# Kernel tuning notes

Measured on AMD Instinct MI355X. Metric: run time of the kernel, lower is better.

Reference implementation:

```python
import jax, jax.numpy as jnp
import numpy as np

BETA = 0.1
CODEBOOK_SIZE = 32768
EMBED_DIM = 4


def setup_inputs() -> dict:
    key = jax.random.key(0)
    kx, ke = jax.random.split(key)
    x = jax.random.normal(kx, (1, 2, EMBED_DIM, 64, 64), dtype=jnp.float32)
    # codebook init mirrors uniform(-1/K, 1/K) but scale doesn't affect correctness;
    # use normal scaled small to keep distances well-conditioned
    E = jax.random.uniform(ke, (CODEBOOK_SIZE, EMBED_DIM), dtype=jnp.float32,
                           minval=-1.0 / CODEBOOK_SIZE, maxval=1.0 / CODEBOOK_SIZE)
    return {"x": x, "E": E}


def reference(x, E):
    b, t, c, h, w = x.shape
    # (B,T,C,H,W) -> (N, C) with N = B*T*H*W
    x_flat = jnp.transpose(x, (0, 1, 3, 4, 2)).reshape(-1, c)
    d = (jnp.sum(x_flat * x_flat, axis=1, keepdims=True)
         + jnp.sum(E * E, axis=1)
         - 2.0 * jnp.einsum('nc,kc->nk', x_flat, E))
    codes = jnp.argmin(d, axis=1)                      # (N,)
    z_q = E[codes].reshape(b, t, h, w, c)              # gather
    z_q = jnp.transpose(z_q, (0, 1, 4, 2, 3))          # (B,T,C,H,W)
    # commitment + codebook loss
    qloss = (jnp.mean((jax.lax.stop_gradient(z_q) - x) ** 2)
             + BETA * jnp.mean((z_q - jax.lax.stop_gradient(x)) ** 2))
    # straight-through estimator
    z_q_st = x + jax.lax.stop_gradient(z_q - x)
    codes = codes.reshape(b, t, h, w)
    return z_q_st, qloss, codes
```

## Files before the change

kernel.cpp:

```cpp
#include <hip/hip_runtime.h>
#include <cfloat>

#define KC    32768
#define NPTS  8192
#define TPB   256
#define PPT   8
#define PTS_PER_BLK (TPB * PPT)
#define NPB   (NPTS / PTS_PER_BLK)
#define NC    256
#define CHUNK (KC / NC)

typedef float v2f __attribute__((ext_vector_type(2)));

template<int H> __device__ __forceinline__ v2f pk_mul_sg(double a, v2f b) {
    v2f d;
    if constexpr (H == 0)
        asm("v_pk_mul_f32 %0, %1, %2 op_sel:[0,0] op_sel_hi:[0,1]" : "=v"(d) : "s"(a), "v"(b));
    else
        asm("v_pk_mul_f32 %0, %1, %2 op_sel:[1,0] op_sel_hi:[1,1]" : "=v"(d) : "s"(a), "v"(b));
    return d;
}
template<int H> __device__ __forceinline__ v2f pk_fma_sg(double a, v2f b, v2f c) {
    v2f d;
    if constexpr (H == 0)
        asm("v_pk_fma_f32 %0, %1, %2, %3 op_sel:[0,0,0] op_sel_hi:[0,1,1]" : "=v"(d) : "s"(a), "v"(b), "v"(c));
    else
        asm("v_pk_fma_f32 %0, %1, %2, %3 op_sel:[1,0,0] op_sel_hi:[1,1,1]" : "=v"(d) : "s"(a), "v"(b), "v"(c));
    return d;
}
template<int H> __device__ __forceinline__ v2f pk_add_sg(double a, v2f b) {
    v2f d;
    if constexpr (H == 0)
        asm("v_pk_add_f32 %0, %1, %2 op_sel:[0,0] op_sel_hi:[0,1]" : "=v"(d) : "s"(a), "v"(b));
    else
        asm("v_pk_add_f32 %0, %1, %2 op_sel:[1,0] op_sel_hi:[1,1]" : "=v"(d) : "s"(a), "v"(b));
    return d;
}
__device__ __forceinline__ v2f pk_add(v2f a, v2f b) {
    v2f d; asm("v_pk_add_f32 %0, %1, %2" : "=v"(d) : "v"(a), "v"(b)); return d;
}
__device__ __forceinline__ float min3f(float a, float b, float c) {
    float d; asm("v_min3_f32 %0, %1, %2, %3" : "=v"(d) : "v"(a), "v"(b), "v"(c)); return d;
}

__global__ __launch_bounds__(256) void k_prep(const float* __restrict__ E,
                                              float* __restrict__ ec) {
#pragma clang fp contract(off)
    const int k = blockIdx.x * 256 + threadIdx.x;
    float4 e = ((const float4*)E)[k];
    ec[k]          = e.x;
    ec[KC + k]     = e.y;
    ec[2 * KC + k] = e.z;
    ec[3 * KC + k] = e.w;
    ec[4 * KC + k] = ((e.x * e.x + e.y * e.y) + e.z * e.z) + e.w * e.w;
}

__global__ __launch_bounds__(TPB) void k_dist(const float* __restrict__ x,
                                              const float* __restrict__ ec,
                                              float* __restrict__ dmn) {
#pragma clang fp contract(off)
    const double* E0 = (const double*)(ec);
    const double* E1 = (const double*)(ec + KC);
    const double* E2 = (const double*)(ec + 2 * KC);
    const double* E3 = (const double*)(ec + 3 * KC);
    const double* Bb = (const double*)(ec + 4 * KC);

    const int chunk = blockIdx.x;
    const int pblk  = blockIdx.y;
    const int tid   = threadIdx.x;
    const int kb2   = chunk * (CHUNK / 2);

    v2f Xm0[4], Xm1[4], Xm2[4], Xm3[4], Aab[4];
#pragma unroll
    for (int u = 0; u < 4; ++u) {
        float xs[2][4], aa[2];
#pragma unroll
        for (int h = 0; h < 2; ++h) {
            const int i = 2 * u + h;
            const int p = pblk * PTS_PER_BLK + i * TPB + tid;
            const int t = p >> 12, s = p & 4095;
            const int xb = t * 16384 + s;
            const float x0 = x[xb], x1 = x[xb + 4096], x2 = x[xb + 8192], x3 = x[xb + 12288];
            xs[h][0] = x0; xs[h][1] = x1; xs[h][2] = x2; xs[h][3] = x3;
            aa[h] = ((x0 * x0 + x1 * x1) + x2 * x2) + x3 * x3;
        }
        Xm0[u] = v2f{-2.0f * xs[0][0], -2.0f * xs[1][0]};
        Xm1[u] = v2f{-2.0f * xs[0][1], -2.0f * xs[1][1]};
        Xm2[u] = v2f{-2.0f * xs[0][2], -2.0f * xs[1][2]};
        Xm3[u] = v2f{-2.0f * xs[0][3], -2.0f * xs[1][3]};
        Aab[u] = v2f{aa[0], aa[1]};
    }

    float bdA[4], bdB[4];
#pragma unroll
    for (int u = 0; u < 4; ++u) { bdA[u] = FLT_MAX; bdB[u] = FLT_MAX; }

#pragma unroll 4
    for (int q = 0; q < CHUNK / 2; ++q) {
        const double se0 = E0[kb2 + q];
        const double se1 = E1[kb2 + q];
        const double se2 = E2[kb2 + q];
        const double se3 = E3[kb2 + q];
        const double sb  = Bb[kb2 + q];
#pragma unroll
        for (int u = 0; u < 4; ++u) {
            v2f m0 = pk_fma_sg<0>(se3, Xm3[u], pk_fma_sg<0>(se2, Xm2[u],
                      pk_fma_sg<0>(se1, Xm1[u], pk_mul_sg<0>(se0, Xm0[u]))));
            v2f t0 = pk_add_sg<0>(sb, Aab[u]);
            v2f d0 = pk_add(m0, t0);
            v2f m1 = pk_fma_sg<1>(se3, Xm3[u], pk_fma_sg<1>(se2, Xm2[u],
                      pk_fma_sg<1>(se1, Xm1[u], pk_mul_sg<1>(se0, Xm0[u]))));
            v2f t1 = pk_add_sg<1>(sb, Aab[u]);
            v2f d1 = pk_add(m1, t1);
            bdA[u] = min3f(bdA[u], d0.x, d1.x);
            bdB[u] = min3f(bdB[u], d0.y, d1.y);
        }
    }
#pragma unroll
    for (int u = 0; u < 4; ++u) {
        const int pA = pblk * PTS_PER_BLK + (2 * u) * TPB + tid;
        const int pB = pblk * PTS_PER_BLK + (2 * u + 1) * TPB + tid;
        dmn[chunk * NPTS + pA] = bdA[u];
        dmn[chunk * NPTS + pB] = bdB[u];
    }
}

__global__ __launch_bounds__(256) void k_merge(const float* __restrict__ x,
                                               const float* __restrict__ E,
                                               const float* __restrict__ dmn,
                                               float* __restrict__ out,
                                               double* __restrict__ partials) {
#pragma clang fp contract(off)
    const int tid  = threadIdx.x;
    const int sub  = tid & 7;
    const int pidx = tid >> 3;
    const int p    = blockIdx.x * 32 + pidx;
    const int t    = p >> 12, s = p & 4095;
    const int xb   = t * 16384 + s;

    const float x0 = x[xb];
    const float x1 = x[xb + 4096];
    const float x2 = x[xb + 8192];
    const float x3 = x[xb + 12288];
    const float a  = ((x0 * x0 + x1 * x1) + x2 * x2) + x3 * x3;

    float bd = FLT_MAX;
    int   bc = 0x7fffffff;
#pragma unroll 8
    for (int i = 0; i < NC / 8; ++i) {
        const int c = sub + 8 * i;
        float d = dmn[c * NPTS + p];
        if (d < bd) { bd = d; bc = c; }
    }
#pragma unroll
    for (int m = 1; m <= 4; m <<= 1) {
        float d2 = __shfl_xor(bd, m);
        int   c2 = __shfl_xor(bc, m);
        if (d2 < bd || (d2 == bd && c2 < bc)) { bd = d2; bc = c2; }
    }

    const int kb = bc * CHUNK;
    int jloc = 1 << 30;
    for (int jj = 0; jj < CHUNK / 8; ++jj) {
        const int j = sub * (CHUNK / 8) + jj;
        float4 e = ((const float4*)E)[kb + j];
        float bn = ((e.x * e.x + e.y * e.y) + e.z * e.z) + e.w * e.w;
        float m_ = __builtin_fmaf(x3, e.w, __builtin_fmaf(x2, e.z,
                    __builtin_fmaf(x1, e.y, x0 * e.x)));
        float t_ = a + bn;
        float d_ = __builtin_fmaf(-2.0f, m_, t_);
        if (d_ == bd) jloc = min(jloc, j);
    }
#pragma unroll
    for (int m = 1; m <= 4; m <<= 1) jloc = min(jloc, __shfl_xor(jloc, m));
    const int bk = kb + (jloc & (CHUNK - 1));

    double ls = 0.0;
    if (sub < 4) {
        const int ch  = sub;
        const int idx = xb + ch * 4096;
        float xv   = x[idx];
        float ev   = E[bk * 4 + ch];
        float diff = ev - xv;
        float sq   = diff * diff;
        out[idx]   = xv + diff;
        ls = (double)sq;
        if (ch == 0) out[32769 + p] = (float)bk;
    }
#pragma unroll
    for (int m = 1; m < 64; m <<= 1) ls += __shfl_xor(ls, m);
    __shared__ double sred[4];
    if ((tid & 63) == 0) sred[tid >> 6] = ls;
    __syncthreads();
    if (tid == 0) partials[blockIdx.x] = sred[0] + sred[1] + sred[2] + sred[3];
}

__global__ void k_loss(const double* __restrict__ partials,
                       float* __restrict__ out) {
#pragma clang fp contract(off)
    if (threadIdx.x == 0 && blockIdx.x == 0) {
        double sum = 0.0;
        for (int i = 0; i < 256; ++i) sum += partials[i];
        float mu = (float)(sum * (1.0 / 32768.0));
        float q  = mu + 0.1f * mu;
        out[32768] = q;
    }
}

extern "C" void kernel_launch(void* const* d_in, const int* in_sizes, int n_in,
                              void* d_out, int out_size, void* d_ws, size_t ws_size,
                              hipStream_t stream) {
    const float* x = (const float*)d_in[0];
    const float* E = (const float*)d_in[1];
    float* out = (float*)d_out;

    char* ws = (char*)d_ws;
    double* partials = (double*)ws;
    float*  ec       = (float*)(ws + 2048);
    float*  dmn      = (float*)(ws + 2048 + 5 * KC * 4);

    k_prep<<<KC / 256, 256, 0, stream>>>(E, ec);
    dim3 g(NC, NPB);
    k_dist<<<g, TPB, 0, stream>>>(x, ec, dmn);
    k_merge<<<NPTS / 32, 256, 0, stream>>>(x, E, dmn, out, partials);
    k_loss<<<1, 64, 0, stream>>>(partials, out);
}
```

Before: 55.85 us.

## Replace packed-FP32 multi-point distance loop with scalar one-point-per-thread kernel

The distance kernel drops the hand-written v_pk_fma inline asm and the 8-points-per-thread register blocking. Each thread now handles one point with scalar FMAs and reads codebook values as scalar floats, and the grid grows from 4 to 32 point-blocks per chunk. This lowers register pressure and raises parallelism. The cost is that every codebook scalar load is amortised over only one point instead of eight, and the packed-math throughput is lost.

New measurement: 99.16 us. 77.5% more time.

```diff
diff --git a/kernel.cpp b/kernel.cpp
--- a/kernel.cpp
+++ b/kernel.cpp
@@ -3,42 +3,9 @@
 
 #define KC    32768
 #define NPTS  8192
-#define TPB   256
-#define PPT   8
-#define PTS_PER_BLK (TPB * PPT)
-#define NPB   (NPTS / PTS_PER_BLK)
 #define NC    256
 #define CHUNK (KC / NC)
 
-typedef float v2f __attribute__((ext_vector_type(2)));
-
-template<int H> __device__ __forceinline__ v2f pk_mul_sg(double a, v2f b) {
-    v2f d;
-    if constexpr (H == 0)
-        asm("v_pk_mul_f32 %0, %1, %2 op_sel:[0,0] op_sel_hi:[0,1]" : "=v"(d) : "s"(a), "v"(b));
-    else
-        asm("v_pk_mul_f32 %0, %1, %2 op_sel:[1,0] op_sel_hi:[1,1]" : "=v"(d) : "s"(a), "v"(b));
-    return d;
-}
-template<int H> __device__ __forceinline__ v2f pk_fma_sg(double a, v2f b, v2f c) {
-    v2f d;
-    if constexpr (H == 0)
-        asm("v_pk_fma_f32 %0, %1, %2, %3 op_sel:[0,0,0] op_sel_hi:[0,1,1]" : "=v"(d) : "s"(a), "v"(b), "v"(c));
-    else
-        asm("v_pk_fma_f32 %0, %1, %2, %3 op_sel:[1,0,0] op_sel_hi:[1,1,1]" : "=v"(d) : "s"(a), "v"(b), "v"(c));
-    return d;
-}
-template<int H> __device__ __forceinline__ v2f pk_add_sg(double a, v2f b) {
-    v2f d;
-    if constexpr (H == 0)
-        asm("v_pk_add_f32 %0, %1, %2 op_sel:[0,0] op_sel_hi:[0,1]" : "=v"(d) : "s"(a), "v"(b));
-    else
-        asm("v_pk_add_f32 %0, %1, %2 op_sel:[1,0] op_sel_hi:[1,1]" : "=v"(d) : "s"(a), "v"(b));
-    return d;
-}
-__device__ __forceinline__ v2f pk_add(v2f a, v2f b) {
-    v2f d; asm("v_pk_add_f32 %0, %1, %2" : "=v"(d) : "v"(a), "v"(b)); return d;
-}
 __device__ __forceinline__ float min3f(float a, float b, float c) {
     float d; asm("v_min3_f32 %0, %1, %2, %3" : "=v"(d) : "v"(a), "v"(b), "v"(c)); return d;
 }
@@ -55,74 +22,49 @@
     ec[4 * KC + k] = ((e.x * e.x + e.y * e.y) + e.z * e.z) + e.w * e.w;
 }
 
-__global__ __launch_bounds__(TPB) void k_dist(const float* __restrict__ x,
+__global__ __launch_bounds__(256) void k_dist(const float* __restrict__ x,
                                               const float* __restrict__ ec,
                                               float* __restrict__ dmn) {
 #pragma clang fp contract(off)
-    const double* E0 = (const double*)(ec);
-    const double* E1 = (const double*)(ec + KC);
-    const double* E2 = (const double*)(ec + 2 * KC);
-    const double* E3 = (const double*)(ec + 3 * KC);
-    const double* Bb = (const double*)(ec + 4 * KC);
+    const float* E0 = ec;
+    const float* E1 = ec + KC;
+    const float* E2 = ec + 2 * KC;
+    const float* E3 = ec + 3 * KC;
+    const float* Bb = ec + 4 * KC;
 
     const int chunk = blockIdx.x;
-    const int pblk  = blockIdx.y;
     const int tid   = threadIdx.x;
-    const int kb2   = chunk * (CHUNK / 2);
+    const int p     = blockIdx.y * 256 + tid;
+    const int kb    = chunk * CHUNK;
 
-    v2f Xm0[4], Xm1[4], Xm2[4], Xm3[4], Aab[4];
-#pragma unroll
-    for (int u = 0; u < 4; ++u) {
-        float xs[2][4], aa[2];
-#pragma unroll
-        for (int h = 0; h < 2; ++h) {
-            const int i = 2 * u + h;
-            const int p = pblk * PTS_PER_BLK + i * TPB + tid;
-            const int t = p >> 12, s = p & 4095;
-            const int xb = t * 16384 + s;
-            const float x0 = x[xb], x1 = x[xb + 4096], x2 = x[xb + 8192], x3 = x[xb + 12288];
-            xs[h][0] = x0; xs[h][1] = x1; xs[h][2] = x2; xs[h][3] = x3;
-            aa[h] = ((x0 * x0 + x1 * x1) + x2 * x2) + x3 * x3;
-        }
-        Xm0[u] = v2f{-2.0f * xs[0][0], -2.0f * xs[1][0]};
-        Xm1[u] = v2f{-2.0f * xs[0][1], -2.0f * xs[1][1]};
-        Xm2[u] = v2f{-2.0f * xs[0][2], -2.0f * xs[1][2]};
-        Xm3[u] = v2f{-2.0f * xs[0][3], -2.0f * xs[1][3]};
-        Aab[u] = v2f{aa[0], aa[1]};
+    const int t  = p >> 12, s = p & 4095;
+    const int xb = t * 16384 + s;
+    const float x0 = x[xb];
+    const float x1 = x[xb + 4096];
+    const float x2 = x[xb + 8192];
+    const float x3 = x[xb + 12288];
+    const float a  = ((x0 * x0 + x1 * x1) + x2 * x2) + x3 * x3;
+    const float xm0 = -2.0f * x0, xm1 = -2.0f * x1;
+    const float xm2 = -2.0f * x2, xm3 = -2.0f * x3;
+
+    float bd = FLT_MAX;
+#pragma unroll 4
+    for (int q = 0; q < CHUNK; q += 2) {
+        const float e00 = E0[kb + q],     e01 = E0[kb + q + 1];
+        const float e10 = E1[kb + q],     e11 = E1[kb + q + 1];
+        const float e20 = E2[kb + q],     e21 = E2[kb + q + 1];
+        const float e30 = E3[kb + q],     e31 = E3[kb + q + 1];
+        const float b0  = Bb[kb + q],     b1  = Bb[kb + q + 1];
+
+        float mm0 = __builtin_fmaf(xm3, e30, __builtin_fmaf(xm2, e20,
+                     __builtin_fmaf(xm1, e10, xm0 * e00)));
+        float d0  = (a + b0) + mm0;
+        float mm1 = __builtin_fmaf(xm3, e31, __builtin_fmaf(xm2, e21,
+                     __builtin_fmaf(xm1, e11, xm0 * e01)));
+        float d1  = (a + b1) + mm1;
+        bd = min3f(bd, d0, d1);
     }
-
-    float bdA[4], bdB[4];
-#pragma unroll
-    for (int u = 0; u < 4; ++u) { bdA[u] = FLT_MAX; bdB[u] = FLT_MAX; }
-
-#pragma unroll 4
-    for (int q = 0; q < CHUNK / 2; ++q) {
-        const double se0 = E0[kb2 + q];
-        const double se1 = E1[kb2 + q];
-        const double se2 = E2[kb2 + q];
-        const double se3 = E3[kb2 + q];
-        const double sb  = Bb[kb2 + q];
-#pragma unroll
-        for (int u = 0; u < 4; ++u) {
-            v2f m0 = pk_fma_sg<0>(se3, Xm3[u], pk_fma_sg<0>(se2, Xm2[u],
-                      pk_fma_sg<0>(se1, Xm1[u], pk_mul_sg<0>(se0, Xm0[u]))));
-            v2f t0 = pk_add_sg<0>(sb, Aab[u]);
-            v2f d0 = pk_add(m0, t0);
-            v2f m1 = pk_fma_sg<1>(se3, Xm3[u], pk_fma_sg<1>(se2, Xm2[u],
-                      pk_fma_sg<1>(se1, Xm1[u], pk_mul_sg<1>(se0, Xm0[u]))));
-            v2f t1 = pk_add_sg<1>(sb, Aab[u]);
-            v2f d1 = pk_add(m1, t1);
-            bdA[u] = min3f(bdA[u], d0.x, d1.x);
-            bdB[u] = min3f(bdB[u], d0.y, d1.y);
-        }
-    }
-#pragma unroll
-    for (int u = 0; u < 4; ++u) {
-        const int pA = pblk * PTS_PER_BLK + (2 * u) * TPB + tid;
-        const int pB = pblk * PTS_PER_BLK + (2 * u + 1) * TPB + tid;
-        dmn[chunk * NPTS + pA] = bdA[u];
-        dmn[chunk * NPTS + pB] = bdB[u];
-    }
+    dmn[chunk * NPTS + p] = bd;
 }
 
 __global__ __launch_bounds__(256) void k_merge(const float* __restrict__ x,
@@ -220,8 +162,8 @@
     float*  dmn      = (float*)(ws + 2048 + 5 * KC * 4);
 
     k_prep<<<KC / 256, 256, 0, stream>>>(E, ec);
-    dim3 g(NC, NPB);
-    k_dist<<<g, TPB, 0, stream>>>(x, ec, dmn);
+    dim3 g(NC, NPTS / 256);
+    k_dist<<<g, 256, 0, stream>>>(x, ec, dmn);
     k_merge<<<NPTS / 32, 256, 0, stream>>>(x, E, dmn, out, partials);
     k_loss<<<1, 64, 0, stream>>>(partials, out);
 }
```
